# Performance work log

Measured on AMD Instinct MI355X. Metric: run time of the kernel, lower is better.

## Reference

```python
import jax, jax.numpy as jnp
import numpy as np

B, S, D, H = 4, 2048, 1024, 16
DH = D // H


def setup_inputs() -> dict:
    key = jax.random.key(0)
    k1, k2, k3, k4, k5 = jax.random.split(key, 5)
    x = jax.random.normal(k1, (B, S, D), dtype=jnp.float32)
    mask = jnp.tril(jnp.ones((S, S), dtype=bool))  # causal mask
    scale = 1.0 / np.sqrt(D)
    w_qkv = jax.random.normal(k2, (D, 3 * D), dtype=jnp.float32) * scale
    b_qkv = jnp.zeros((3 * D,), dtype=jnp.float32)
    w_out = jax.random.normal(k3, (D, D), dtype=jnp.float32) * scale
    b_out = jnp.zeros((D,), dtype=jnp.float32)
    return {"x": x, "w_qkv": w_qkv, "b_qkv": b_qkv, "w_out": w_out, "b_out": b_out, "mask": mask}


def reference(x, w_qkv, b_qkv, w_out, b_out, mask):
    qkv = jnp.einsum('bsd,de->bse', x, w_qkv) + b_qkv  # (B,S,3D)
    q, k, v = jnp.split(qkv, 3, axis=-1)
    # (B,S,D) -> (B,H,S,DH)
    q = q.reshape(B, S, H, DH).transpose(0, 2, 1, 3)
    k = k.reshape(B, S, H, DH).transpose(0, 2, 1, 3)
    v = v.reshape(B, S, H, DH).transpose(0, 2, 1, 3)
    scores = jnp.einsum('bhqd,bhkd->bhqk', q, k) / jnp.sqrt(jnp.float32(DH))
    scores = jnp.where(mask[None, None, :, :], scores, -jnp.inf)
    attn = jax.nn.softmax(scores, axis=-1)  # dropout p=0.0 -> identity
    out = jnp.einsum('bhqk,bhkd->bhqd', attn, v)
    out = out.transpose(0, 2, 1, 3).reshape(B, S, D)
    return jnp.einsum('bsd,de->bse', out, w_out) + b_out
```

## Files before the change

### kernel.cpp

```cpp
#include <hip/hip_runtime.h>
#include <hip/hip_bf16.h>

typedef unsigned short u16;
typedef __bf16 bf16x8 __attribute__((ext_vector_type(8)));
typedef float f32x4 __attribute__((ext_vector_type(4)));
typedef unsigned short u16x8 __attribute__((ext_vector_type(8)));

__device__ __forceinline__ void async_copy16(void* lds, const void* g) {
  __builtin_amdgcn_global_load_lds(
      (const __attribute__((address_space(1))) unsigned int*)g,
      (__attribute__((address_space(3))) unsigned int*)lds, 16, 0, 0);
}

__device__ __forceinline__ u16 f2bf(float f) {
  __hip_bfloat16 h = __float2bfloat16(f);
  u16 u;
  __builtin_memcpy(&u, &h, 2);
  return u;
}

__device__ __forceinline__ u16 f2bf_rne(float f) {
  unsigned b = __builtin_bit_cast(unsigned, f);
  b += 0x7FFF + ((b >> 16) & 1);
  return (u16)(b >> 16);
}

__device__ __forceinline__ unsigned cvt_pk_bf16(float a, float b) {
  unsigned r;
  asm("v_cvt_pk_bf16_f32 %0, %1, %2" : "=v"(r) : "v"(a), "v"(b));
  return r;
}

__global__ void k_f32_to_bf16(const float* __restrict__ in, u16* __restrict__ out, int n4) {
  int i = blockIdx.x * blockDim.x + threadIdx.x;
  if (i >= n4) return;
  float4 v = ((const float4*)in)[i];
  ushort4 o;
  o.x = f2bf(v.x); o.y = f2bf(v.y); o.z = f2bf(v.z); o.w = f2bf(v.w);
  ((ushort4*)out)[i] = o;
}

__global__ void k_transpose_bf16(const float* __restrict__ in, u16* __restrict__ out, int R, int C) {
  __shared__ float tile[32][33];
  int bx = blockIdx.x * 32;
  int by = blockIdx.y * 32;
  int tx = threadIdx.x & 31, ty = threadIdx.x >> 5;
  for (int i = ty; i < 32; i += 8) tile[i][tx] = in[(size_t)(by + i) * C + bx + tx];
  __syncthreads();
  for (int i = ty; i < 32; i += 8) out[(size_t)(bx + i) * R + by + tx] = f2bf(tile[tx][i]);
}

template <int OUT_BF16>
__global__ __launch_bounds__(256, 2) void k_gemm_bt(
    const u16* __restrict__ A, const u16* __restrict__ Bt,
    const float* __restrict__ bias, void* __restrict__ Cout,
    int M, int N, int K) {
  __shared__ __align__(16) u16 As[128][32];
  __shared__ __align__(16) u16 Bs[128][32];
  const int t = threadIdx.x;
  const int l = t & 63, w = t >> 6;
  const int lr = l & 15, lk = l >> 4;
  const int wr = w >> 1, wc = w & 1;
  const int m0 = blockIdx.x * 128, n0 = blockIdx.y * 128;

  f32x4 acc[4][4] = {};

  for (int k0 = 0; k0 < K; k0 += 32) {
    __syncthreads();
    for (int c = 0; c < 2; ++c) {
      int idx = c * 256 + t;
      int row = idx >> 2, slot = idx & 3;
      int sw = (slot ^ ((row >> 1) & 3)) << 3;
      async_copy16((char*)&As[0][0] + idx * 16, A + (size_t)(m0 + row) * K + k0 + sw);
      async_copy16((char*)&Bs[0][0] + idx * 16, Bt + (size_t)(n0 + row) * K + k0 + sw);
    }
    __syncthreads();
    bf16x8 af[4], bfr[4];
    for (int m = 0; m < 4; ++m) {
      int row = wr * 64 + m * 16 + lr;
      af[m] = *(const bf16x8*)((const char*)&As[0][0] + row * 64 + ((lk ^ ((row >> 1) & 3)) << 4));
    }
    for (int n = 0; n < 4; ++n) {
      int row = wc * 64 + n * 16 + lr;
      bfr[n] = *(const bf16x8*)((const char*)&Bs[0][0] + row * 64 + ((lk ^ ((row >> 1) & 3)) << 4));
    }
    for (int m = 0; m < 4; ++m)
      for (int n = 0; n < 4; ++n)
        acc[m][n] = __builtin_amdgcn_mfma_f32_16x16x32_bf16(af[m], bfr[n], acc[m][n], 0, 0, 0);
  }

  for (int n = 0; n < 4; ++n) {
    int col = n0 + wc * 64 + n * 16 + lr;
    float bv = bias[col];
    for (int m = 0; m < 4; ++m) {
      int rowb = m0 + wr * 64 + m * 16 + lk * 4;
      for (int r = 0; r < 4; ++r) {
        float v = acc[m][n][r] + bv;
        size_t off = (size_t)(rowb + r) * N + col;
        if constexpr (OUT_BF16) ((u16*)Cout)[off] = f2bf(v);
        else ((float*)Cout)[off] = v;
      }
    }
  }
}

__global__ __launch_bounds__(256, 3) void k_attn(
    const u16* __restrict__ QKV,
    u16* __restrict__ O) {
  const int bh = blockIdx.x;
  const int p = blockIdx.y;
  const int b = bh >> 4, h = bh & 15;
  const int t = threadIdx.x;
  const int l = t & 63, w = t >> 6;
  const int lr = l & 15, lk = l >> 4;
  constexpr float LG = 0.18033688f;

  __shared__ __align__(16) u16 Ks[2][64][64];
  __shared__ __align__(16) u16 VT[2][64][64];
  __shared__ __align__(16) u16 Pl[4][32][64];

  const u16* Kb0 = QKV + (size_t)b * 2048 * 3072 + 1024 + h * 64;
  const u16* Vb0 = Kb0 + 1024;

  u16x8 vreg[2];

  auto stageK = [&](int j, int buf) {
#pragma unroll
    for (int c = 0; c < 2; ++c) {
      int gi = c * 256 + t;
      int row = gi >> 3, slot = gi & 7;
      async_copy16((char*)&Ks[buf][0][0] + gi * 16,
                   Kb0 + ((size_t)j * 64 + row) * 3072 + ((slot ^ (row & 7)) << 3));
    }
  };
  auto loadV = [&](int j) {
#pragma unroll
    for (int c = 0; c < 2; ++c) {
      int r = c * 32 + (t >> 3), dh0 = (t & 7) << 3;
      vreg[c] = *(const u16x8*)(Vb0 + ((size_t)j * 64 + r) * 3072 + dh0);
    }
  };
  auto writeV = [&](int buf) {
#pragma unroll
    for (int c = 0; c < 2; ++c) {
      int r = c * 32 + (t >> 3), dh0 = (t & 7) << 3;
#pragma unroll
      for (int jj = 0; jj < 8; ++jj) {
        int dh = dh0 + jj;
        int phi = (dh & 7) ^ ((dh >> 3) & 7);
        VT[buf][dh][((((r >> 3) ^ phi) & 7) << 3) | (r & 7)] = vreg[c][jj];
      }
    }
  };

  auto run_tile = [&](int qt) {
    const int nt = 2 * qt + 2;
    const int q0w = qt * 128 + w * 32;
    const size_t rowQ = (size_t)b * 2048 + q0w;

    bf16x8 qf[2][2];
#pragma unroll
    for (int g = 0; g < 2; ++g)
#pragma unroll
      for (int c = 0; c < 2; ++c)
        qf[g][c] = *(const bf16x8*)(QKV + (rowQ + g * 16 + lr) * 3072 + h * 64 + c * 32 + lk * 8);

    f32x4 acc[2][4] = {};
    float mi[2], li[2];
#pragma unroll
    for (int g = 0; g < 2; ++g) { mi[g] = -__builtin_inff(); li[g] = 0.f; }

    stageK(0, 0);
    loadV(0);
    writeV(0);
    __syncthreads();

    for (int j = 0; j < nt; ++j) {
      const int cur = j & 1;
      const bool more = (j + 1 < nt);
      if (more) { stageK(j + 1, cur ^ 1); loadV(j + 1); }

      f32x4 s[2][4] = {};
#pragma unroll
      for (int c = 0; c < 2; ++c)
#pragma unroll
        for (int n = 0; n < 4; ++n) {
          int row = n * 16 + lr;
          bf16x8 kf = *(const bf16x8*)((const char*)&Ks[cur][0][0] + row * 128 +
                                       ((((c * 4 + lk) ^ (row & 7)) & 7) << 4));
          s[0][n] = __builtin_amdgcn_mfma_f32_16x16x32_bf16(kf, qf[0][c], s[0][n], 0, 0, 0);
          s[1][n] = __builtin_amdgcn_mfma_f32_16x16x32_bf16(kf, qf[1][c], s[1][n], 0, 0, 0);
        }

      if (j * 64 + 63 > q0w) {
        const int kb = j * 64 + lk * 4;
#pragma unroll
        for (int g = 0; g < 2; ++g) {
          const int qq = q0w + g * 16 + lr;
#pragma unroll
          for (int n = 0; n < 4; ++n)
#pragma unroll
            for (int r = 0; r < 4; ++r)
              if (kb + n * 16 + r > qq) s[g][n][r] = -__builtin_inff();
        }
      }

      float tm[2];
#pragma unroll
      for (int g = 0; g < 2; ++g) {
        float m0 = fmaxf(fmaxf(s[g][0][0], s[g][0][1]), fmaxf(s[g][0][2], s[g][0][3]));
        float m1 = fmaxf(fmaxf(s[g][1][0], s[g][1][1]), fmaxf(s[g][1][2], s[g][1][3]));
        float m2 = fmaxf(fmaxf(s[g][2][0], s[g][2][1]), fmaxf(s[g][2][2], s[g][2][3]));
        float m3 = fmaxf(fmaxf(s[g][3][0], s[g][3][1]), fmaxf(s[g][3][2], s[g][3][3]));
        float x = fmaxf(fmaxf(m0, m1), fmaxf(m2, m3));
        x = fmaxf(x, __shfl_xor(x, 16));
        x = fmaxf(x, __shfl_xor(x, 32));
        tm[g] = x;
      }
      if (__any((tm[0] > mi[0] + 64.0f) || (tm[1] > mi[1] + 64.0f))) {
#pragma unroll
        for (int g = 0; g < 2; ++g) {
          float mnew = fmaxf(mi[g], tm[g]);
          float alpha = __builtin_amdgcn_exp2f((mi[g] - mnew) * LG);
          mi[g] = mnew;
          li[g] *= alpha;
          float a0 = __shfl(alpha, lk * 4 + 0);
          float a1 = __shfl(alpha, lk * 4 + 1);
          float a2 = __shfl(alpha, lk * 4 + 2);
          float a3 = __shfl(alpha, lk * 4 + 3);
#pragma unroll
          for (int n = 0; n < 4; ++n) {
            acc[g][n][0] *= a0; acc[g][n][1] *= a1; acc[g][n][2] *= a2; acc[g][n][3] *= a3;
          }
        }
      }

      u16* pw = &Pl[w][0][0];
#pragma unroll
      for (int g = 0; g < 2; ++g) {
        const float mc = -mi[g] * LG;
        float ps = 0.f;
#pragma unroll
        for (int n = 0; n < 4; ++n) {
          float p0 = __builtin_amdgcn_exp2f(fmaf(s[g][n][0], LG, mc));
          float p1 = __builtin_amdgcn_exp2f(fmaf(s[g][n][1], LG, mc));
          float p2 = __builtin_amdgcn_exp2f(fmaf(s[g][n][2], LG, mc));
          float p3 = __builtin_amdgcn_exp2f(fmaf(s[g][n][3], LG, mc));
          ps += (p0 + p1) + (p2 + p3);
          unsigned w0 = cvt_pk_bf16(p0, p1);
          unsigned w1 = cvt_pk_bf16(p2, p3);
          int kc = (n * 2 + (lk >> 1)) ^ (lr & 7);
          *(uint2*)(pw + (g * 16 + lr) * 64 + kc * 8 + (lk & 1) * 4) = make_uint2(w0, w1);
        }
        ps += __shfl_xor(ps, 16);
        ps += __shfl_xor(ps, 32);
        li[g] += ps;
      }

#pragma unroll
      for (int c = 0; c < 2; ++c) {
        bf16x8 pa0 = *(const bf16x8*)(pw + lr * 64 + (((c * 4 + lk) ^ (lr & 7)) << 3));
        bf16x8 pa1 = *(const bf16x8*)(pw + (16 + lr) * 64 + (((c * 4 + lk) ^ (lr & 7)) << 3));
#pragma unroll
        for (int n = 0; n < 4; ++n) {
          int dh = n * 16 + lr;
          int phi = (dh & 7) ^ ((dh >> 3) & 7);
          bf16x8 vf = *(const bf16x8*)((const char*)&VT[cur][0][0] + dh * 128 +
                                       ((((c * 4 + lk) ^ phi) & 7) << 4));
          acc[0][n] = __builtin_amdgcn_mfma_f32_16x16x32_bf16(pa0, vf, acc[0][n], 0, 0, 0);
          acc[1][n] = __builtin_amdgcn_mfma_f32_16x16x32_bf16(pa1, vf, acc[1][n], 0, 0, 0);
        }
      }

      if (more) writeV(cur ^ 1);
      __syncthreads();
    }

#pragma unroll
    for (int g = 0; g < 2; ++g) {
      float l0 = __shfl(li[g], lk * 4 + 0);
      float l1 = __shfl(li[g], lk * 4 + 1);
      float l2 = __shfl(li[g], lk * 4 + 2);
      float l3 = __shfl(li[g], lk * 4 + 3);
      float inv[4] = {1.0f / l0, 1.0f / l1, 1.0f / l2, 1.0f / l3};
#pragma unroll
      for (int r = 0; r < 4; ++r) {
        size_t orow = (rowQ + g * 16 + lk * 4 + r) * 1024 + h * 64;
#pragma unroll
        for (int n = 0; n < 4; ++n) O[orow + n * 16 + lr] = f2bf_rne(acc[g][n][r] * inv[r]);
      }
    }
  };

  run_tile(15 - p);
  run_tile(p);
}

extern "C" void kernel_launch(void* const* d_in, const int* in_sizes, int n_in,
                              void* d_out, int out_size, void* d_ws, size_t ws_size,
                              hipStream_t stream) {
  const float* x = (const float*)d_in[0];
  const float* w_qkv = (const float*)d_in[1];
  const float* b_qkv = (const float*)d_in[2];
  const float* w_out = (const float*)d_in[3];
  const float* b_out = (const float*)d_in[4];

  char* ws = (char*)d_ws;
  u16* X16 = (u16*)(ws);
  u16* WqkvT = (u16*)(ws + 16777216);
  u16* WoutT = (u16*)(ws + 23068672);
  u16* QKVb = (u16*)(ws + 25165824);
  u16* O16 = X16;

  k_f32_to_bf16<<<8192, 256, 0, stream>>>(x, X16, 8388608 / 4);
  k_transpose_bf16<<<dim3(96, 32), 256, 0, stream>>>(w_qkv, WqkvT, 1024, 3072);
  k_transpose_bf16<<<dim3(32, 32), 256, 0, stream>>>(w_out, WoutT, 1024, 1024);
  k_gemm_bt<1><<<dim3(64, 24), 256, 0, stream>>>(X16, WqkvT, b_qkv, QKVb, 8192, 3072, 1024);
  k_attn<<<dim3(64, 8), 256, 0, stream>>>(QKVb, O16);
  k_gemm_bt<0><<<dim3(64, 8), 256, 0, stream>>>(O16, WoutT, b_out, d_out, 8192, 1024, 1024);
}
```

Baseline: 185.7 us.

## Use 512-thread attention blocks with one 256-row query tile each

The attention kernel changes from 4 waves each running two 128-row query tiles (paired for causal balance) to 8 waves running a single 256-row query tile. This halves K/V staging per wave, since each K/V tile is shared by twice as many query rows. Blocks are issued in a descending-then-ascending order of work via a lookup table. s_setprio is raised around the MFMA sections. The risks are a loss of the causal pairing balance, which can leave per-block work uneven across the grid, and a larger LDS footprint for P.

```diff
diff --git a/kernel.cpp b/kernel.cpp
--- a/kernel.cpp
+++ b/kernel.cpp
@@ -104,11 +104,12 @@
   }
 }
 
-__global__ __launch_bounds__(256, 3) void k_attn(
+__global__ __launch_bounds__(512, 4) void k_attn(
     const u16* __restrict__ QKV,
     u16* __restrict__ O) {
   const int bh = blockIdx.x;
-  const int p = blockIdx.y;
+  const int qmap[8] = {7, 5, 3, 1, 0, 2, 4, 6};
+  const int qt = qmap[blockIdx.y];
   const int b = bh >> 4, h = bh & 15;
   const int t = threadIdx.x;
   const int l = t & 63, w = t >> 6;
@@ -117,183 +118,171 @@
 
   __shared__ __align__(16) u16 Ks[2][64][64];
   __shared__ __align__(16) u16 VT[2][64][64];
-  __shared__ __align__(16) u16 Pl[4][32][64];
+  __shared__ __align__(16) u16 Pl[8][32][64];
 
   const u16* Kb0 = QKV + (size_t)b * 2048 * 3072 + 1024 + h * 64;
   const u16* Vb0 = Kb0 + 1024;
 
-  u16x8 vreg[2];
+  u16x8 vreg;
 
   auto stageK = [&](int j, int buf) {
-#pragma unroll
-    for (int c = 0; c < 2; ++c) {
-      int gi = c * 256 + t;
-      int row = gi >> 3, slot = gi & 7;
-      async_copy16((char*)&Ks[buf][0][0] + gi * 16,
-                   Kb0 + ((size_t)j * 64 + row) * 3072 + ((slot ^ (row & 7)) << 3));
-    }
+    int row = t >> 3, slot = t & 7;
+    async_copy16((char*)&Ks[buf][0][0] + t * 16,
+                 Kb0 + ((size_t)j * 64 + row) * 3072 + ((slot ^ (row & 7)) << 3));
   };
   auto loadV = [&](int j) {
-#pragma unroll
-    for (int c = 0; c < 2; ++c) {
-      int r = c * 32 + (t >> 3), dh0 = (t & 7) << 3;
-      vreg[c] = *(const u16x8*)(Vb0 + ((size_t)j * 64 + r) * 3072 + dh0);
-    }
+    vreg = *(const u16x8*)(Vb0 + ((size_t)j * 64 + (t >> 3)) * 3072 + ((t & 7) << 3));
   };
   auto writeV = [&](int buf) {
+    int r = t >> 3, dh0 = (t & 7) << 3;
+#pragma unroll
+    for (int jj = 0; jj < 8; ++jj) {
+      int dh = dh0 + jj;
+      int phi = (dh & 7) ^ ((dh >> 3) & 7);
+      VT[buf][dh][((((r >> 3) ^ phi) & 7) << 3) | (r & 7)] = vreg[jj];
+    }
+  };
+
+  const int nt = 4 * qt + 4;
+  const int q0w = qt * 256 + w * 32;
+  const size_t rowQ = (size_t)b * 2048 + q0w;
+
+  bf16x8 qf[2][2];
+#pragma unroll
+  for (int g = 0; g < 2; ++g)
+#pragma unroll
+    for (int c = 0; c < 2; ++c)
+      qf[g][c] = *(const bf16x8*)(QKV + (rowQ + g * 16 + lr) * 3072 + h * 64 + c * 32 + lk * 8);
+
+  f32x4 acc[2][4] = {};
+  float mi[2], li[2];
+#pragma unroll
+  for (int g = 0; g < 2; ++g) { mi[g] = -__builtin_inff(); li[g] = 0.f; }
+
+  stageK(0, 0);
+  loadV(0);
+  writeV(0);
+  __syncthreads();
+
+  for (int j = 0; j < nt; ++j) {
+    const int cur = j & 1;
+    const bool more = (j + 1 < nt);
+    if (more) { stageK(j + 1, cur ^ 1); loadV(j + 1); }
+
+    f32x4 s[2][4] = {};
+    __builtin_amdgcn_s_setprio(1);
+#pragma unroll
+    for (int c = 0; c < 2; ++c)
+#pragma unroll
+      for (int n = 0; n < 4; ++n) {
+        int row = n * 16 + lr;
+        bf16x8 kf = *(const bf16x8*)((const char*)&Ks[cur][0][0] + row * 128 +
+                                     ((((c * 4 + lk) ^ (row & 7)) & 7) << 4));
+        s[0][n] = __builtin_amdgcn_mfma_f32_16x16x32_bf16(kf, qf[0][c], s[0][n], 0, 0, 0);
+        s[1][n] = __builtin_amdgcn_mfma_f32_16x16x32_bf16(kf, qf[1][c], s[1][n], 0, 0, 0);
+      }
+    __builtin_amdgcn_s_setprio(0);
+
+    if (j * 64 + 63 > q0w) {
+      const int kb = j * 64 + lk * 4;
+#pragma unroll
+      for (int g = 0; g < 2; ++g) {
+        const int qq = q0w + g * 16 + lr;
+#pragma unroll
+        for (int n = 0; n < 4; ++n)
+#pragma unroll
+          for (int r = 0; r < 4; ++r)
+            if (kb + n * 16 + r > qq) s[g][n][r] = -__builtin_inff();
+      }
+    }
+
+    float tm[2];
+#pragma unroll
+    for (int g = 0; g < 2; ++g) {
+      float m0 = fmaxf(fmaxf(s[g][0][0], s[g][0][1]), fmaxf(s[g][0][2], s[g][0][3]));
+      float m1 = fmaxf(fmaxf(s[g][1][0], s[g][1][1]), fmaxf(s[g][1][2], s[g][1][3]));
+      float m2 = fmaxf(fmaxf(s[g][2][0], s[g][2][1]), fmaxf(s[g][2][2], s[g][2][3]));
+      float m3 = fmaxf(fmaxf(s[g][3][0], s[g][3][1]), fmaxf(s[g][3][2], s[g][3][3]));
+      float x = fmaxf(fmaxf(m0, m1), fmaxf(m2, m3));
+      x = fmaxf(x, __shfl_xor(x, 16));
+      x = fmaxf(x, __shfl_xor(x, 32));
+      tm[g] = x;
+    }
+    if (__any((tm[0] > mi[0] + 64.0f) || (tm[1] > mi[1] + 64.0f))) {
+#pragma unroll
+      for (int g = 0; g < 2; ++g) {
+        float mnew = fmaxf(mi[g], tm[g]);
+        float alpha = __builtin_amdgcn_exp2f((mi[g] - mnew) * LG);
+        mi[g] = mnew;
+        li[g] *= alpha;
+        float a0 = __shfl(alpha, lk * 4 + 0);
+        float a1 = __shfl(alpha, lk * 4 + 1);
+        float a2 = __shfl(alpha, lk * 4 + 2);
+        float a3 = __shfl(alpha, lk * 4 + 3);
+#pragma unroll
+        for (int n = 0; n < 4; ++n) {
+          acc[g][n][0] *= a0; acc[g][n][1] *= a1; acc[g][n][2] *= a2; acc[g][n][3] *= a3;
+        }
+      }
+    }
+
+    u16* pw = &Pl[w][0][0];
+#pragma unroll
+    for (int g = 0; g < 2; ++g) {
+      const float mc = -mi[g] * LG;
+      float ps = 0.f;
+#pragma unroll
+      for (int n = 0; n < 4; ++n) {
+        float p0 = __builtin_amdgcn_exp2f(fmaf(s[g][n][0], LG, mc));
+        float p1 = __builtin_amdgcn_exp2f(fmaf(s[g][n][1], LG, mc));
+        float p2 = __builtin_amdgcn_exp2f(fmaf(s[g][n][2], LG, mc));
+        float p3 = __builtin_amdgcn_exp2f(fmaf(s[g][n][3], LG, mc));
+        ps += (p0 + p1) + (p2 + p3);
+        unsigned w0 = cvt_pk_bf16(p0, p1);
+        unsigned w1 = cvt_pk_bf16(p2, p3);
+        int kc = (n * 2 + (lk >> 1)) ^ (lr & 7);
+        *(uint2*)(pw + (g * 16 + lr) * 64 + kc * 8 + (lk & 1) * 4) = make_uint2(w0, w1);
+      }
+      ps += __shfl_xor(ps, 16);
+      ps += __shfl_xor(ps, 32);
+      li[g] += ps;
+    }
+
+    __builtin_amdgcn_s_setprio(1);
 #pragma unroll
     for (int c = 0; c < 2; ++c) {
-      int r = c * 32 + (t >> 3), dh0 = (t & 7) << 3;
-#pragma unroll
-      for (int jj = 0; jj < 8; ++jj) {
-        int dh = dh0 + jj;
+      bf16x8 pa0 = *(const bf16x8*)(pw + lr * 64 + (((c * 4 + lk) ^ (lr & 7)) << 3));
+      bf16x8 pa1 = *(const bf16x8*)(pw + (16 + lr) * 64 + (((c * 4 + lk) ^ (lr & 7)) << 3));
+#pragma unroll
+      for (int n = 0; n < 4; ++n) {
+        int dh = n * 16 + lr;
         int phi = (dh & 7) ^ ((dh >> 3) & 7);
-        VT[buf][dh][((((r >> 3) ^ phi) & 7) << 3) | (r & 7)] = vreg[c][jj];
-      }
-    }
-  };
-
-  auto run_tile = [&](int qt) {
-    const int nt = 2 * qt + 2;
-    const int q0w = qt * 128 + w * 32;
-    const size_t rowQ = (size_t)b * 2048 + q0w;
-
-    bf16x8 qf[2][2];
-#pragma unroll
-    for (int g = 0; g < 2; ++g)
-#pragma unroll
-      for (int c = 0; c < 2; ++c)
-        qf[g][c] = *(const bf16x8*)(QKV + (rowQ + g * 16 + lr) * 3072 + h * 64 + c * 32 + lk * 8);
-
-    f32x4 acc[2][4] = {};
-    float mi[2], li[2];
-#pragma unroll
-    for (int g = 0; g < 2; ++g) { mi[g] = -__builtin_inff(); li[g] = 0.f; }
-
-    stageK(0, 0);
-    loadV(0);
-    writeV(0);
+        bf16x8 vf = *(const bf16x8*)((const char*)&VT[cur][0][0] + dh * 128 +
+                                     ((((c * 4 + lk) ^ phi) & 7) << 4));
+        acc[0][n] = __builtin_amdgcn_mfma_f32_16x16x32_bf16(pa0, vf, acc[0][n], 0, 0, 0);
+        acc[1][n] = __builtin_amdgcn_mfma_f32_16x16x32_bf16(pa1, vf, acc[1][n], 0, 0, 0);
+      }
+    }
+    __builtin_amdgcn_s_setprio(0);
+
+    if (more) writeV(cur ^ 1);
     __syncthreads();
-
-    for (int j = 0; j < nt; ++j) {
-      const int cur = j & 1;
-      const bool more = (j + 1 < nt);
-      if (more) { stageK(j + 1, cur ^ 1); loadV(j + 1); }
-
-      f32x4 s[2][4] = {};
-#pragma unroll
-      for (int c = 0; c < 2; ++c)
-#pragma unroll
-        for (int n = 0; n < 4; ++n) {
-          int row = n * 16 + lr;
-          bf16x8 kf = *(const bf16x8*)((const char*)&Ks[cur][0][0] + row * 128 +
-                                       ((((c * 4 + lk) ^ (row & 7)) & 7) << 4));
-          s[0][n] = __builtin_amdgcn_mfma_f32_16x16x32_bf16(kf, qf[0][c], s[0][n], 0, 0, 0);
-          s[1][n] = __builtin_amdgcn_mfma_f32_16x16x32_bf16(kf, qf[1][c], s[1][n], 0, 0, 0);
-        }
-
-      if (j * 64 + 63 > q0w) {
-        const int kb = j * 64 + lk * 4;
-#pragma unroll
-        for (int g = 0; g < 2; ++g) {
-          const int qq = q0w + g * 16 + lr;
-#pragma unroll
-          for (int n = 0; n < 4; ++n)
-#pragma unroll
-            for (int r = 0; r < 4; ++r)
-              if (kb + n * 16 + r > qq) s[g][n][r] = -__builtin_inff();
-        }
-      }
-
-      float tm[2];
-#pragma unroll
-      for (int g = 0; g < 2; ++g) {
-        float m0 = fmaxf(fmaxf(s[g][0][0], s[g][0][1]), fmaxf(s[g][0][2], s[g][0][3]));
-        float m1 = fmaxf(fmaxf(s[g][1][0], s[g][1][1]), fmaxf(s[g][1][2], s[g][1][3]));
-        float m2 = fmaxf(fmaxf(s[g][2][0], s[g][2][1]), fmaxf(s[g][2][2], s[g][2][3]));
-        float m3 = fmaxf(fmaxf(s[g][3][0], s[g][3][1]), fmaxf(s[g][3][2], s[g][3][3]));
-        float x = fmaxf(fmaxf(m0, m1), fmaxf(m2, m3));
-        x = fmaxf(x, __shfl_xor(x, 16));
-        x = fmaxf(x, __shfl_xor(x, 32));
-        tm[g] = x;
-      }
-      if (__any((tm[0] > mi[0] + 64.0f) || (tm[1] > mi[1] + 64.0f))) {
-#pragma unroll
-        for (int g = 0; g < 2; ++g) {
-          float mnew = fmaxf(mi[g], tm[g]);
-          float alpha = __builtin_amdgcn_exp2f((mi[g] - mnew) * LG);
-          mi[g] = mnew;
-          li[g] *= alpha;
-          float a0 = __shfl(alpha, lk * 4 + 0);
-          float a1 = __shfl(alpha, lk * 4 + 1);
-          float a2 = __shfl(alpha, lk * 4 + 2);
-          float a3 = __shfl(alpha, lk * 4 + 3);
-#pragma unroll
-          for (int n = 0; n < 4; ++n) {
-            acc[g][n][0] *= a0; acc[g][n][1] *= a1; acc[g][n][2] *= a2; acc[g][n][3] *= a3;
-          }
-        }
-      }
-
-      u16* pw = &Pl[w][0][0];
-#pragma unroll
-      for (int g = 0; g < 2; ++g) {
-        const float mc = -mi[g] * LG;
-        float ps = 0.f;
-#pragma unroll
-        for (int n = 0; n < 4; ++n) {
-          float p0 = __builtin_amdgcn_exp2f(fmaf(s[g][n][0], LG, mc));
-          float p1 = __builtin_amdgcn_exp2f(fmaf(s[g][n][1], LG, mc));
-          float p2 = __builtin_amdgcn_exp2f(fmaf(s[g][n][2], LG, mc));
-          float p3 = __builtin_amdgcn_exp2f(fmaf(s[g][n][3], LG, mc));
-          ps += (p0 + p1) + (p2 + p3);
-          unsigned w0 = cvt_pk_bf16(p0, p1);
-          unsigned w1 = cvt_pk_bf16(p2, p3);
-          int kc = (n * 2 + (lk >> 1)) ^ (lr & 7);
-          *(uint2*)(pw + (g * 16 + lr) * 64 + kc * 8 + (lk & 1) * 4) = make_uint2(w0, w1);
-        }
-        ps += __shfl_xor(ps, 16);
-        ps += __shfl_xor(ps, 32);
-        li[g] += ps;
-      }
-
-#pragma unroll
-      for (int c = 0; c < 2; ++c) {
-        bf16x8 pa0 = *(const bf16x8*)(pw + lr * 64 + (((c * 4 + lk) ^ (lr & 7)) << 3));
-        bf16x8 pa1 = *(const bf16x8*)(pw + (16 + lr) * 64 + (((c * 4 + lk) ^ (lr & 7)) << 3));
-#pragma unroll
-        for (int n = 0; n < 4; ++n) {
-          int dh = n * 16 + lr;
-          int phi = (dh & 7) ^ ((dh >> 3) & 7);
-          bf16x8 vf = *(const bf16x8*)((const char*)&VT[cur][0][0] + dh * 128 +
-                                       ((((c * 4 + lk) ^ phi) & 7) << 4));
-          acc[0][n] = __builtin_amdgcn_mfma_f32_16x16x32_bf16(pa0, vf, acc[0][n], 0, 0, 0);
-          acc[1][n] = __builtin_amdgcn_mfma_f32_16x16x32_bf16(pa1, vf, acc[1][n], 0, 0, 0);
-        }
-      }
-
-      if (more) writeV(cur ^ 1);
-      __syncthreads();
-    }
-
-#pragma unroll
-    for (int g = 0; g < 2; ++g) {
-      float l0 = __shfl(li[g], lk * 4 + 0);
-      float l1 = __shfl(li[g], lk * 4 + 1);
-      float l2 = __shfl(li[g], lk * 4 + 2);
-      float l3 = __shfl(li[g], lk * 4 + 3);
-      float inv[4] = {1.0f / l0, 1.0f / l1, 1.0f / l2, 1.0f / l3};
-#pragma unroll
-      for (int r = 0; r < 4; ++r) {
-        size_t orow = (rowQ + g * 16 + lk * 4 + r) * 1024 + h * 64;
-#pragma unroll
-        for (int n = 0; n < 4; ++n) O[orow + n * 16 + lr] = f2bf_rne(acc[g][n][r] * inv[r]);
-      }
-    }
-  };
-
-  run_tile(15 - p);
-  run_tile(p);
+  }
+
+#pragma unroll
+  for (int g = 0; g < 2; ++g) {
+    float l0 = __shfl(li[g], lk * 4 + 0);
+    float l1 = __shfl(li[g], lk * 4 + 1);
+    float l2 = __shfl(li[g], lk * 4 + 2);
+    float l3 = __shfl(li[g], lk * 4 + 3);
+    float inv[4] = {1.0f / l0, 1.0f / l1, 1.0f / l2, 1.0f / l3};
+#pragma unroll
+    for (int r = 0; r < 4; ++r) {
+      size_t orow = (rowQ + g * 16 + lk * 4 + r) * 1024 + h * 64;
+#pragma unroll
+      for (int n = 0; n < 4; ++n) O[orow + n * 16 + lr] = f2bf_rne(acc[g][n][r] * inv[r]);
+    }
+  }
 }
 
 extern "C" void kernel_launch(void* const* d_in, const int* in_sizes, int n_in,
@@ -316,6 +305,6 @@
   k_transpose_bf16<<<dim3(96, 32), 256, 0, stream>>>(w_qkv, WqkvT, 1024, 3072);
   k_transpose_bf16<<<dim3(32, 32), 256, 0, stream>>>(w_out, WoutT, 1024, 1024);
   k_gemm_bt<1><<<dim3(64, 24), 256, 0, stream>>>(X16, WqkvT, b_qkv, QKVb, 8192, 3072, 1024);
-  k_attn<<<dim3(64, 8), 256, 0, stream>>>(QKVb, O16);
+  k_attn<<<dim3(64, 8), 512, 0, stream>>>(QKVb, O16);
   k_gemm_bt<0><<<dim3(64, 8), 256, 0, stream>>>(O16, WoutT, b_out, d_out, 8192, 1024, 1024);
 }
```

New measurement: 234.3 us. 1.26x slower.
